# Kernel tuning notes

Measured on AMD Instinct MI355X. Metric: run time of the kernel, lower is better.

The kernel has to match this reference:

```python
import jax, jax.numpy as jnp
import numpy as np
import math

D_RES, N_HEADS, D_HEAD, D_MLP = 1024, 16, 64, 4096
EPS = 1e-5
IGNORE = -100000.0


def setup_inputs() -> dict:
    key = jax.random.key(0)
    ks = jax.random.split(key, 8)
    std = 0.02
    return {
        "resid_pre": jax.random.normal(ks[0], (2, 2048, D_RES), dtype=jnp.float32),
        "ln1_w": jnp.ones((D_RES,), jnp.float32),
        "ln1_b": jnp.zeros((D_RES,), jnp.float32),
        "W_Q": jax.random.normal(ks[1], (N_HEADS, D_RES, D_HEAD), jnp.float32) * std,
        "b_Q": jnp.zeros((N_HEADS, D_HEAD), jnp.float32),
        "W_K": jax.random.normal(ks[2], (N_HEADS, D_RES, D_HEAD), jnp.float32) * std,
        "b_K": jnp.zeros((N_HEADS, D_HEAD), jnp.float32),
        "W_V": jax.random.normal(ks[3], (N_HEADS, D_RES, D_HEAD), jnp.float32) * std,
        "b_V": jnp.zeros((N_HEADS, D_HEAD), jnp.float32),
        "W_O": jax.random.normal(ks[4], (N_HEADS, D_HEAD, D_RES), jnp.float32) * std,
        "b_O": jnp.zeros((D_RES,), jnp.float32),
        "ln2_w": jnp.ones((D_RES,), jnp.float32),
        "ln2_b": jnp.zeros((D_RES,), jnp.float32),
        "W_in": jax.random.normal(ks[5], (D_RES, D_MLP), jnp.float32) * std,
        "b_in": jnp.zeros((D_MLP,), jnp.float32),
        "W_out": jax.random.normal(ks[6], (D_MLP, D_RES), jnp.float32) * std,
        "b_out": jnp.zeros((D_RES,), jnp.float32),
    }


def _layernorm(x, w, b):
    x = x - jnp.mean(x, axis=-1, keepdims=True)
    scale = jnp.sqrt(jnp.mean(x * x, axis=-1, keepdims=True) + EPS)
    return (x / scale) * w + b


def reference(resid_pre, ln1_w, ln1_b, W_Q, b_Q, W_K, b_K, W_V, b_V, W_O, b_O,
              ln2_w, ln2_b, W_in, b_in, W_out, b_out):
    x = _layernorm(resid_pre, ln1_w, ln1_b)  # [b,s,d]
    q = jnp.einsum('bsd,hde->bshe', x, W_Q) + b_Q
    k = jnp.einsum('bsd,hde->bshe', x, W_K) + b_K
    v = jnp.einsum('bsd,hde->bshe', x, W_V) + b_V
    scores = jnp.einsum('bqhe,bkhe->bhqk', q, k) / math.sqrt(D_HEAD)
    S = scores.shape[-1]
    mask = jnp.triu(jnp.ones((S, S), dtype=bool), k=1)
    scores = jnp.where(mask, IGNORE, scores)
    pattern = jax.nn.softmax(scores, axis=-1)
    z = jnp.einsum('bhqk,bkhe->bqhe', pattern, v)
    attn_out = jnp.einsum('bqhe,hed->bqd', z, W_O) + b_O
    resid_mid = resid_pre + attn_out
    y = _layernorm(resid_mid, ln2_w, ln2_b)
    pre = jnp.einsum('bsd,dm->bsm', y, W_in) + b_in
    post = jax.nn.gelu(pre, approximate=False)
    mlp_out = jnp.einsum('bsm,md->bsd', post, W_out) + b_out
    return resid_mid + mlp_out
```

## Files before the change

kernel.cpp:

```cpp
#include <hip/hip_runtime.h>
#include <cstddef>

typedef unsigned short u16;
using short8 = __attribute__((ext_vector_type(8))) short;
using f32x4  = __attribute__((ext_vector_type(4))) float;

__device__ __forceinline__ float bf2f(u16 u) {
  union { unsigned int i; float f; } v; v.i = ((unsigned int)u) << 16; return v.f;
}
__device__ __forceinline__ u16 f2bf(float f) {
  __bf16 h = (__bf16)f;
  return __builtin_bit_cast(unsigned short, h);
}

__device__ __forceinline__ void load_lds16(const u16* g, u16* l) {
  __builtin_amdgcn_global_load_lds((const __attribute__((address_space(1))) void*)g,
                                   (__attribute__((address_space(3))) void*)l, 16, 0, 0);
}

__global__ __launch_bounds__(256) void transpose_k(const float* __restrict__ in,
                                                   u16* __restrict__ out,
                                                   int R, int C,
                                                   long inB, long outB) {
  __shared__ float tile[32][33];
  long zb = blockIdx.z;
  in  += zb * inB;
  out += zb * outB;
  int c0 = blockIdx.x * 32, r0 = blockIdx.y * 32;
  int tx = threadIdx.x, ty = threadIdx.y;
#pragma unroll
  for (int i = 0; i < 32; i += 8)
    tile[ty + i][tx] = in[(long)(r0 + ty + i) * C + c0 + tx];
  __syncthreads();
#pragma unroll
  for (int i = 0; i < 32; i += 8)
    out[(long)(c0 + ty + i) * R + r0 + tx] = f2bf(tile[tx][ty + i]);
}

__global__ __launch_bounds__(256) void transpose_v_k(const u16* __restrict__ qkv,
                                                     u16* __restrict__ vT) {
  __shared__ u16 tile[32][33];
  int bh = blockIdx.z;
  int b = bh >> 4, h = bh & 15;
  const u16* in = qkv + (size_t)b * 2048 * 3072 + 2048 + h * 64;
  u16* out = vT + (size_t)bh * 64 * 2048;
  int e0 = blockIdx.x * 32, s0 = blockIdx.y * 32;
  int tx = threadIdx.x, ty = threadIdx.y;
#pragma unroll
  for (int i = 0; i < 32; i += 8)
    tile[ty + i][tx] = in[(size_t)(s0 + ty + i) * 3072 + e0 + tx];
  __syncthreads();
#pragma unroll
  for (int i = 0; i < 32; i += 8)
    out[(size_t)(e0 + ty + i) * 2048 + s0 + tx] = tile[tx][ty + i];
}

__global__ void build_qkv_bias(const float* __restrict__ bQ, const float* __restrict__ bK,
                               const float* __restrict__ bV, float* __restrict__ out) {
  int i = blockIdx.x * 256 + threadIdx.x;
  float v;
  if (i < 1024) v = bQ[i];
  else if (i < 2048) v = bK[i - 1024];
  else v = bV[i - 2048];
  out[i] = v;
}

__global__ __launch_bounds__(256) void ln_k(const float* __restrict__ inp,
                                            const float* __restrict__ w,
                                            const float* __restrict__ bias,
                                            u16* __restrict__ out) {
  __shared__ float red[2][4];
  int row = blockIdx.x, t = threadIdx.x;
  int wave = t >> 6, lane = t & 63;
  size_t base = (size_t)row * 1024 + t * 4;
  float4 f = *(const float4*)(inp + base);
  float v[4] = {f.x, f.y, f.z, f.w};
  float s = v[0] + v[1] + v[2] + v[3];
#pragma unroll
  for (int off = 32; off; off >>= 1) s += __shfl_xor(s, off, 64);
  if (lane == 0) red[0][wave] = s;
  __syncthreads();
  float mean = (red[0][0] + red[0][1] + red[0][2] + red[0][3]) * (1.f / 1024.f);
  float c[4]; float sq = 0.f;
#pragma unroll
  for (int j = 0; j < 4; ++j) { c[j] = v[j] - mean; sq += c[j] * c[j]; }
#pragma unroll
  for (int off = 32; off; off >>= 1) sq += __shfl_xor(sq, off, 64);
  if (lane == 0) red[1][wave] = sq;
  __syncthreads();
  float var = (red[1][0] + red[1][1] + red[1][2] + red[1][3]) * (1.f / 1024.f);
  float inv = 1.f / sqrtf(var + 1e-5f);
  float4 wv = *(const float4*)(w + t * 4);
  float4 bv = *(const float4*)(bias + t * 4);
  out[base + 0] = f2bf(c[0] * inv * wv.x + bv.x);
  out[base + 1] = f2bf(c[1] * inv * wv.y + bv.y);
  out[base + 2] = f2bf(c[2] * inv * wv.z + bv.z);
  out[base + 3] = f2bf(c[3] * inv * wv.w + bv.w);
}

template<int TN, bool RESIDF, bool GELU, bool OUTF32>
__global__ __launch_bounds__(256, 2) void gemm_k(const u16* __restrict__ A,
                                                 const u16* __restrict__ BT,
                                                 const float* __restrict__ bias,
                                                 const float* __restrict__ resid,
                                                 void* __restrict__ Cout,
                                                 int M, int N, int K) {
  constexpr int NS = TN / 32;
  __shared__ u16 As[128 * 64];
  __shared__ u16 Bs[TN * 64];
  int n0 = blockIdx.x * TN, m0 = blockIdx.y * 128;
  int t = threadIdx.x;
  int wave = t >> 6, lane = t & 63;
  int wr = wave >> 1, wc = wave & 1;
  int ln16 = lane & 15, quad = lane >> 4;

  f32x4 acc[4][NS];
#pragma unroll
  for (int i = 0; i < 4; ++i)
#pragma unroll
    for (int j = 0; j < NS; ++j) acc[i][j] = (f32x4){0.f, 0.f, 0.f, 0.f};

  int lrow8 = lane >> 3;
  int gseg  = (lane & 7) ^ lrow8;
  const u16* aG = A  + (size_t)(m0 + wave * 8 + lrow8) * K + gseg * 8;
  const u16* bG = BT + (size_t)(n0 + wave * 8 + lrow8) * K + gseg * 8;
  u16* aL = As + wave * 8 * 64;
  u16* bL = Bs + wave * 8 * 64;

  int e = ln16 & 7;
  int arow = wr * 64 + ln16;
  int brow = wc * (TN / 2) + ln16;

  for (int k0 = 0; k0 < K; k0 += 64) {
    __syncthreads();
#pragma unroll
    for (int i = 0; i < 4; ++i)
      load_lds16(aG + (size_t)i * 32 * K + k0, aL + i * 32 * 64);
#pragma unroll
    for (int i = 0; i < TN / 32; ++i)
      load_lds16(bG + (size_t)i * 32 * K + k0, bL + i * 32 * 64);
    __syncthreads();
#pragma unroll
    for (int kk = 0; kk < 2; ++kk) {
      int slot = (kk * 4 + quad) ^ e;
      short8 af[4], bf[NS];
#pragma unroll
      for (int ms = 0; ms < 4; ++ms)
        af[ms] = *(const short8*)&As[(arow + ms * 16) * 64 + slot * 8];
#pragma unroll
      for (int ns = 0; ns < NS; ++ns)
        bf[ns] = *(const short8*)&Bs[(brow + ns * 16) * 64 + slot * 8];
#pragma unroll
      for (int ms = 0; ms < 4; ++ms)
#pragma unroll
        for (int ns = 0; ns < NS; ++ns)
          acc[ms][ns] = __builtin_amdgcn_mfma_f32_16x16x32_bf16(af[ms], bf[ns], acc[ms][ns], 0, 0, 0);
    }
  }

#pragma unroll
  for (int ms = 0; ms < 4; ++ms)
#pragma unroll
    for (int ns = 0; ns < NS; ++ns)
#pragma unroll
      for (int r = 0; r < 4; ++r) {
        int grow = m0 + wr * 64 + ms * 16 + quad * 4 + r;
        int gcol = n0 + wc * (TN / 2) + ns * 16 + ln16;
        size_t idx = (size_t)grow * N + gcol;
        float v = acc[ms][ns][r] + bias[gcol];
        if (GELU) v = 0.5f * v * (1.f + erff(v * 0.70710678118654752f));
        if (RESIDF) v += resid[idx];
        if (OUTF32) ((float*)Cout)[idx] = v;
        else        ((u16*)Cout)[idx] = f2bf(v);
      }
}

template<bool GELU>
__global__ __launch_bounds__(512, 2) void gemm256_k(const u16* __restrict__ A,
                                                    const u16* __restrict__ BT,
                                                    const float* __restrict__ bias,
                                                    u16* __restrict__ C,
                                                    int M, int N, int K) {
  constexpr int SLOT = 8192;
  __shared__ __align__(16) u16 As[4 * SLOT];
  __shared__ __align__(16) u16 Bs[4 * SLOT];
  int n0 = blockIdx.x * 256, m0 = blockIdx.y * 256;
  int t = threadIdx.x;
  int w = t >> 6, lane = t & 63;
  int wr = w >> 2, wc = w & 3;
  int ln16 = lane & 15, quad = lane >> 4;

  f32x4 acc[8][4];
#pragma unroll
  for (int i = 0; i < 8; ++i)
#pragma unroll
    for (int j = 0; j < 4; ++j) acc[i][j] = (f32x4){0.f, 0.f, 0.f, 0.f};

  const u16* aG0 = A  + (size_t)(m0 + w * 32 + (lane >> 2)) * K + (lane & 3) * 8;
  const u16* bG0 = BT + (size_t)(n0 + w * 32 + (lane >> 2)) * K + (lane & 3) * 8;
  u16* aL0 = As + w * 1024;
  u16* bL0 = Bs + w * 1024;

#define STAGE_A(j, tg) do {                                         \
    const u16* _g = aG0 + (size_t)(j) * 32;                         \
    u16* _l = aL0 + (tg) * SLOT;                                    \
    load_lds16(_g, _l);                                             \
    load_lds16(_g + (size_t)16 * K, _l + 512);                      \
  } while (0)
#define STAGE_B(j, tg) do {                                         \
    const u16* _g = bG0 + (size_t)(j) * 32;                         \
    u16* _l = bL0 + (tg) * SLOT;                                    \
    load_lds16(_g, _l);                                             \
    load_lds16(_g + (size_t)16 * K, _l + 512);                      \
  } while (0)

  STAGE_A(0, 0); STAGE_B(0, 0);
  STAGE_A(1, 1); STAGE_B(1, 1);
  STAGE_A(2, 2); STAGE_B(2, 2);
  asm volatile("s_waitcnt vmcnt(8)" ::: "memory");
  __builtin_amdgcn_s_barrier();

  int nslot = K >> 5;
  const u16* aRd = As + (wr * 128 + ln16) * 32 + quad * 8;
  const u16* bRd = Bs + (wc * 64  + ln16) * 32 + quad * 8;

  for (int s = 0; s < nslot; ++s) {
    int cur = s & 3, tgt = (s + 3) & 3;
    const u16* aB = aRd + cur * SLOT;
    const u16* bB = bRd + cur * SLOT;
    short8 a[4], b[4];

#pragma unroll
    for (int i = 0; i < 4; ++i) a[i] = *(const short8*)(aB + i * 512);
#pragma unroll
    for (int i = 0; i < 4; ++i) b[i] = *(const short8*)(bB + i * 512);
    if (s + 3 < nslot) STAGE_A(s + 3, tgt);
    __builtin_amdgcn_s_barrier();
    __builtin_amdgcn_s_setprio(1);
#pragma unroll
    for (int ms = 0; ms < 4; ++ms)
#pragma unroll
      for (int ns = 0; ns < 4; ++ns)
        acc[ms][ns] = __builtin_amdgcn_mfma_f32_16x16x32_bf16(a[ms], b[ns], acc[ms][ns], 0, 0, 0);
    __builtin_amdgcn_s_setprio(0);
    __builtin_amdgcn_s_barrier();

#pragma unroll
    for (int i = 0; i < 4; ++i) a[i] = *(const short8*)(aB + (4 + i) * 512);
    if (s + 3 < nslot) {
      STAGE_B(s + 3, tgt);
      asm volatile("s_waitcnt vmcnt(8)" ::: "memory");
    } else if (s + 2 < nslot) {
      asm volatile("s_waitcnt vmcnt(4)" ::: "memory");
    } else if (s + 1 < nslot) {
      asm volatile("s_waitcnt vmcnt(0)" ::: "memory");
    }
    __builtin_amdgcn_s_barrier();
    __builtin_amdgcn_s_setprio(1);
#pragma unroll
    for (int ms = 0; ms < 4; ++ms)
#pragma unroll
      for (int ns = 0; ns < 4; ++ns)
        acc[4 + ms][ns] = __builtin_amdgcn_mfma_f32_16x16x32_bf16(a[ms], b[ns], acc[4 + ms][ns], 0, 0, 0);
    __builtin_amdgcn_s_setprio(0);
    __builtin_amdgcn_s_barrier();
  }
#undef STAGE_A
#undef STAGE_B

#pragma unroll
  for (int ms = 0; ms < 8; ++ms)
#pragma unroll
    for (int ns = 0; ns < 4; ++ns) {
      int gcol = n0 + wc * 64 + ns * 16 + ln16;
      float bb = bias[gcol];
#pragma unroll
      for (int r = 0; r < 4; ++r) {
        int grow = m0 + wr * 128 + ms * 16 + quad * 4 + r;
        float v = acc[ms][ns][r] + bb;
        if (GELU) v = 0.5f * v * (1.f + erff(v * 0.70710678118654752f));
        C[(size_t)grow * N + gcol] = f2bf(v);
      }
    }
}

__global__ __launch_bounds__(512) void attn_k(const u16* __restrict__ qkv,
                                              const u16* __restrict__ vT,
                                              u16* __restrict__ z) {
  __shared__ __align__(16) u16 Ks[3 * 8192];
  __shared__ __align__(16) u16 Vs[3 * 8192];
  __shared__ __align__(16) u16 Ps[8 * 2048];
  int bh = blockIdx.x, p = blockIdx.y;
  int b = bh >> 4, h = bh & 15;
  int tA = p, tB = 15 - p;
  int t = threadIdx.x, w = t >> 6, lane = t & 63;
  int ln16 = lane & 15, quad = lane >> 4, e = ln16 & 7;

  short8 aq[2][2];
#pragma unroll
  for (int ti = 0; ti < 2; ++ti) {
    int tq = ti ? tB : tA;
    const u16* qrow = qkv + (size_t)(b * 2048 + tq * 128 + w * 16 + ln16) * 3072 + h * 64;
    aq[ti][0] = *(const short8*)(qrow + quad * 8);
    aq[ti][1] = *(const short8*)(qrow + 32 + quad * 8);
  }

  f32x4 zero4 = {0.f, 0.f, 0.f, 0.f};
  f32x4 o[2][4];
  float l_i[2][4];
#pragma unroll
  for (int ti = 0; ti < 2; ++ti)
#pragma unroll
    for (int n = 0; n < 4; ++n) { o[ti][n] = zero4; l_i[ti][n] = 0.f; }

  const u16* kB = qkv + (size_t)(b * 2048 + w * 16 + (lane >> 3)) * 3072
                + 1024 + h * 64 + (((lane & 7) ^ (lane >> 3))) * 8;
  const u16* vB0 = vT + ((size_t)(b * 16 + h) * 64 + w * 8 + (lane >> 4)) * 2048
                 + (((lane & 15) ^ (lane >> 4))) * 8;
  const u16* vB1 = vT + ((size_t)(b * 16 + h) * 64 + w * 8 + 4 + (lane >> 4)) * 2048
                 + (((lane & 15) ^ (4 + (lane >> 4)))) * 8;
  u16* kL = Ks + w * 16 * 64;
  u16* vL = Vs + w * 8 * 128;
  u16* psW = Ps + w * 2048;

#define STAGE(kt_, rg_) do {                                              \
    size_t kOff = (size_t)(kt_) * 128 * 3072;                             \
    u16* _kl = kL + (rg_) * 8192;                                         \
    load_lds16(kB + kOff, _kl);                                           \
    load_lds16(kB + kOff + (size_t)8 * 3072, _kl + 8 * 64);               \
    size_t vOff = (size_t)(kt_) * 128;                                    \
    u16* _vl = vL + (rg_) * 8192;                                         \
    load_lds16(vB0 + vOff, _vl);                                          \
    load_lds16(vB1 + vOff, _vl + 4 * 128);                                \
  } while (0)

  int nkt = tB + 1;
  STAGE(0, 0);

  for (int kt = 0; kt < nkt; ++kt) {
    int ring = kt % 3;
    if (kt + 1 < nkt) {
      STAGE(kt + 1, (kt + 1) % 3);
      asm volatile("s_waitcnt vmcnt(4)" ::: "memory");
    } else {
      asm volatile("s_waitcnt vmcnt(0)" ::: "memory");
    }
    __builtin_amdgcn_s_barrier();

    const u16* ks = Ks + ring * 8192;
    const u16* vs = Vs + ring * 8192;
    int kg = kt * 128;

#pragma unroll
    for (int ti = 0; ti < 2; ++ti) {
      int tq = ti ? tB : tA;
      if (kt > tq) continue;

      f32x4 s[8] = {zero4, zero4, zero4, zero4, zero4, zero4, zero4, zero4};
#pragma unroll
      for (int kk = 0; kk < 2; ++kk) {
        short8 a = aq[ti][kk];
        int slot = (kk * 4 + quad) ^ e;
#pragma unroll
        for (int n = 0; n < 8; ++n) {
          short8 kb = *(const short8*)&ks[(n * 16 + ln16) * 64 + slot * 8];
          s[n] = __builtin_amdgcn_mfma_f32_16x16x32_bf16(a, kb, s[n], 0, 0, 0);
        }
      }

      bool diag = (kt == tq);
      int qgb = tq * 128 + w * 16 + quad * 4;
#pragma unroll
      for (int r = 0; r < 4; ++r) {
        int q = quad * 4 + r, q7 = q & 7;
        int gq = qgb + r;
        float psum = 0.f;
#pragma unroll
        for (int n = 0; n < 8; ++n) {
          float pv = __expf(s[n][r] * 0.125f);
          if (diag && (kg + n * 16 + ln16 > gq)) pv = 0.f;
          psum += pv;
          psW[q * 128 + ((((n << 1) | (ln16 >> 3)) ^ q7) << 3) + e] = f2bf(pv);
        }
        l_i[ti][r] += psum;
      }

#pragma unroll
      for (int kk = 0; kk < 4; ++kk) {
        int slot = (kk * 4 + quad) ^ e;
        short8 ap = *(const short8*)&psW[ln16 * 128 + slot * 8];
#pragma unroll
        for (int n = 0; n < 4; ++n) {
          short8 bv = *(const short8*)&vs[(n * 16 + ln16) * 128 + slot * 8];
          o[ti][n] = __builtin_amdgcn_mfma_f32_16x16x32_bf16(ap, bv, o[ti][n], 0, 0, 0);
        }
      }
    }
  }
#undef STAGE

#pragma unroll
  for (int ti = 0; ti < 2; ++ti) {
    int tq = ti ? tB : tA;
    float inv[4];
#pragma unroll
    for (int r = 0; r < 4; ++r) {
      float sum = l_i[ti][r];
#pragma unroll
      for (int off = 8; off; off >>= 1) sum += __shfl_xor(sum, off, 16);
      inv[r] = 1.f / sum;
    }
#pragma unroll
    for (int n = 0; n < 4; ++n)
#pragma unroll
      for (int r = 0; r < 4; ++r)
        z[(size_t)(b * 2048 + tq * 128 + w * 16 + quad * 4 + r) * 1024
          + h * 64 + n * 16 + ln16] = f2bf(o[ti][n][r] * inv[r]);
  }
}

extern "C" void kernel_launch(void* const* d_in, const int* in_sizes, int n_in,
                              void* d_out, int out_size, void* d_ws, size_t ws_size,
                              hipStream_t stream) {
  const float* resid_pre = (const float*)d_in[0];
  const float* ln1_w = (const float*)d_in[1];
  const float* ln1_b = (const float*)d_in[2];
  const float* W_Q  = (const float*)d_in[3];
  const float* b_Q  = (const float*)d_in[4];
  const float* W_K  = (const float*)d_in[5];
  const float* b_K  = (const float*)d_in[6];
  const float* W_V  = (const float*)d_in[7];
  const float* b_V  = (const float*)d_in[8];
  const float* W_O  = (const float*)d_in[9];
  const float* b_O  = (const float*)d_in[10];
  const float* ln2_w = (const float*)d_in[11];
  const float* ln2_b = (const float*)d_in[12];
  const float* W_in  = (const float*)d_in[13];
  const float* b_in  = (const float*)d_in[14];
  const float* W_out = (const float*)d_in[15];
  const float* b_out = (const float*)d_in[16];
  float* out = (float*)d_out;

  char* w = (char*)d_ws;
  u16* WqkvT = (u16*)w;  w += (size_t)3072 * 1024 * 2;
  u16* WoT   = (u16*)w;  w += (size_t)1024 * 1024 * 2;
  u16* WinT  = (u16*)w;  w += (size_t)4096 * 1024 * 2;
  u16* WoutT = (u16*)w;  w += (size_t)1024 * 4096 * 2;
  float* qkvBias = (float*)w; w += 3072 * 4;
  u16* xln   = (u16*)w;  w += (size_t)4096 * 1024 * 2;
  float* resid_mid = (float*)w; w += (size_t)4096 * 1024 * 4;
  u16* qkvBuf = (u16*)w; w += (size_t)4096 * 3072 * 2;
  u16* zBuf  = (u16*)w;  w += (size_t)4096 * 1024 * 2;
  u16* vTBuf = (u16*)w;  w += (size_t)32 * 64 * 2048 * 2;
  u16* hBuf  = qkvBuf;

  dim3 tb(32, 8);
  transpose_k<<<dim3(2, 32, 16), tb, 0, stream>>>(W_Q, WqkvT,                1024, 64, 65536, 65536);
  transpose_k<<<dim3(2, 32, 16), tb, 0, stream>>>(W_K, WqkvT + 1024 * 1024,  1024, 64, 65536, 65536);
  transpose_k<<<dim3(2, 32, 16), tb, 0, stream>>>(W_V, WqkvT + 2048 * 1024,  1024, 64, 65536, 65536);
  transpose_k<<<dim3(32, 32, 1), tb, 0, stream>>>(W_O,  WoT,   1024, 1024, 0, 0);
  transpose_k<<<dim3(128, 32, 1), tb, 0, stream>>>(W_in, WinT,  1024, 4096, 0, 0);
  transpose_k<<<dim3(32, 128, 1), tb, 0, stream>>>(W_out, WoutT, 4096, 1024, 0, 0);
  build_qkv_bias<<<12, 256, 0, stream>>>(b_Q, b_K, b_V, qkvBias);

  ln_k<<<4096, 256, 0, stream>>>(resid_pre, ln1_w, ln1_b, xln);
  gemm256_k<false><<<dim3(12, 16), 512, 0, stream>>>(
      xln, WqkvT, qkvBias, qkvBuf, 4096, 3072, 1024);
  transpose_v_k<<<dim3(2, 64, 32), tb, 0, stream>>>(qkvBuf, vTBuf);
  attn_k<<<dim3(32, 8, 1), 512, 0, stream>>>(qkvBuf, vTBuf, zBuf);
  gemm_k<64, true, false, true><<<dim3(16, 32), 256, 0, stream>>>(
      zBuf, WoT, b_O, resid_pre, resid_mid, 4096, 1024, 1024);
  ln_k<<<4096, 256, 0, stream>>>(resid_mid, ln2_w, ln2_b, xln);
  gemm256_k<true><<<dim3(16, 16), 512, 0, stream>>>(
      xln, WinT, b_in, hBuf, 4096, 4096, 1024);
  gemm_k<64, true, false, true><<<dim3(16, 32), 256, 0, stream>>>(
      hBuf, WoutT, b_out, resid_mid, out, 4096, 1024, 4096);
}
```

Measured before the change: 365.1 us.

## Restructure 256x256 GEMM to double-buffered BK=64 tiles with XOR-swizzled LDS

Reworks the large GEMM's main loop. The old 4-slot ring with K-step 32 and split A/B staging becomes a 2-slot double buffer with K-step 64, one combined stage per iteration, and a single barrier pair per slot. The LDS row layout is XOR-swizzled to avoid bank conflicts when each lane reads 16-byte fragments. This halves the barrier count and the waitcnt bookkeeping per K element, but leaves only one tile of prefetch lookahead where there used to be three, which may expose global-load latency.

```diff
diff --git a/kernel.cpp b/kernel.cpp
--- a/kernel.cpp
+++ b/kernel.cpp
@@ -181,9 +181,9 @@
                                                     const float* __restrict__ bias,
                                                     u16* __restrict__ C,
                                                     int M, int N, int K) {
-  constexpr int SLOT = 8192;
-  __shared__ __align__(16) u16 As[4 * SLOT];
-  __shared__ __align__(16) u16 Bs[4 * SLOT];
+  constexpr int SLOT = 256 * 64;
+  __shared__ __align__(16) u16 As[2 * SLOT];
+  __shared__ __align__(16) u16 Bs[2 * SLOT];
   int n0 = blockIdx.x * 256, m0 = blockIdx.y * 256;
   int t = threadIdx.x;
   int w = t >> 6, lane = t & 63;
@@ -196,77 +196,67 @@
 #pragma unroll
     for (int j = 0; j < 4; ++j) acc[i][j] = (f32x4){0.f, 0.f, 0.f, 0.f};
 
-  const u16* aG0 = A  + (size_t)(m0 + w * 32 + (lane >> 2)) * K + (lane & 3) * 8;
-  const u16* bG0 = BT + (size_t)(n0 + w * 32 + (lane >> 2)) * K + (lane & 3) * 8;
-  u16* aL0 = As + w * 1024;
-  u16* bL0 = Bs + w * 1024;
-
-#define STAGE_A(j, tg) do {                                         \
-    const u16* _g = aG0 + (size_t)(j) * 32;                         \
-    u16* _l = aL0 + (tg) * SLOT;                                    \
-    load_lds16(_g, _l);                                             \
-    load_lds16(_g + (size_t)16 * K, _l + 512);                      \
+  int r8 = t >> 3;
+  int seg = (t & 7) ^ (r8 & 7);
+  const u16* aG0 = A  + (size_t)(m0 + r8) * K + seg * 8;
+  const u16* bG0 = BT + (size_t)(n0 + r8) * K + seg * 8;
+  u16* aLw = As + w * 512;
+  u16* bLw = Bs + w * 512;
+
+#define STAGE(s_, tg_) do {                                              \
+    const u16* _ga = aG0 + (size_t)(s_) * 64;                            \
+    const u16* _gb = bG0 + (size_t)(s_) * 64;                            \
+    u16* _la = aLw + (tg_) * SLOT;                                       \
+    u16* _lb = bLw + (tg_) * SLOT;                                       \
+    load_lds16(_ga,                       _la);                          \
+    load_lds16(_ga + (size_t)64 * K,      _la + 4096);                   \
+    load_lds16(_ga + (size_t)128 * K,     _la + 8192);                   \
+    load_lds16(_ga + (size_t)192 * K,     _la + 12288);                  \
+    load_lds16(_gb,                       _lb);                          \
+    load_lds16(_gb + (size_t)64 * K,      _lb + 4096);                   \
+    load_lds16(_gb + (size_t)128 * K,     _lb + 8192);                   \
+    load_lds16(_gb + (size_t)192 * K,     _lb + 12288);                  \
   } while (0)
-#define STAGE_B(j, tg) do {                                         \
-    const u16* _g = bG0 + (size_t)(j) * 32;                         \
-    u16* _l = bL0 + (tg) * SLOT;                                    \
-    load_lds16(_g, _l);                                             \
-    load_lds16(_g + (size_t)16 * K, _l + 512);                      \
-  } while (0)
-
-  STAGE_A(0, 0); STAGE_B(0, 0);
-  STAGE_A(1, 1); STAGE_B(1, 1);
-  STAGE_A(2, 2); STAGE_B(2, 2);
-  asm volatile("s_waitcnt vmcnt(8)" ::: "memory");
-  __builtin_amdgcn_s_barrier();
-
-  int nslot = K >> 5;
-  const u16* aRd = As + (wr * 128 + ln16) * 32 + quad * 8;
-  const u16* bRd = Bs + (wc * 64  + ln16) * 32 + quad * 8;
+
+  STAGE(0, 0);
+
+  int e = ln16 & 7;
+  int nslot = K >> 6;
+  const u16* aRd = As + (size_t)(wr * 128 + ln16) * 64;
+  const u16* bRd = Bs + (size_t)(wc * 64 + ln16) * 64;
 
   for (int s = 0; s < nslot; ++s) {
-    int cur = s & 3, tgt = (s + 3) & 3;
+    int cur = s & 1;
+    if (s + 1 < nslot) {
+      STAGE(s + 1, cur ^ 1);
+      asm volatile("s_waitcnt vmcnt(8)" ::: "memory");
+    } else {
+      asm volatile("s_waitcnt vmcnt(0)" ::: "memory");
+    }
+    __builtin_amdgcn_s_barrier();
+
     const u16* aB = aRd + cur * SLOT;
     const u16* bB = bRd + cur * SLOT;
-    short8 a[4], b[4];
-
-#pragma unroll
-    for (int i = 0; i < 4; ++i) a[i] = *(const short8*)(aB + i * 512);
-#pragma unroll
-    for (int i = 0; i < 4; ++i) b[i] = *(const short8*)(bB + i * 512);
-    if (s + 3 < nslot) STAGE_A(s + 3, tgt);
-    __builtin_amdgcn_s_barrier();
     __builtin_amdgcn_s_setprio(1);
 #pragma unroll
-    for (int ms = 0; ms < 4; ++ms)
+    for (int kk = 0; kk < 2; ++kk) {
+      int slot = (kk * 4 + quad) ^ e;
+      short8 bf[4];
 #pragma unroll
       for (int ns = 0; ns < 4; ++ns)
-        acc[ms][ns] = __builtin_amdgcn_mfma_f32_16x16x32_bf16(a[ms], b[ns], acc[ms][ns], 0, 0, 0);
-    __builtin_amdgcn_s_setprio(0);
-    __builtin_amdgcn_s_barrier();
-
-#pragma unroll
-    for (int i = 0; i < 4; ++i) a[i] = *(const short8*)(aB + (4 + i) * 512);
-    if (s + 3 < nslot) {
-      STAGE_B(s + 3, tgt);
-      asm volatile("s_waitcnt vmcnt(8)" ::: "memory");
-    } else if (s + 2 < nslot) {
-      asm volatile("s_waitcnt vmcnt(4)" ::: "memory");
-    } else if (s + 1 < nslot) {
-      asm volatile("s_waitcnt vmcnt(0)" ::: "memory");
-    }
-    __builtin_amdgcn_s_barrier();
-    __builtin_amdgcn_s_setprio(1);
-#pragma unroll
-    for (int ms = 0; ms < 4; ++ms)
-#pragma unroll
-      for (int ns = 0; ns < 4; ++ns)
-        acc[4 + ms][ns] = __builtin_amdgcn_mfma_f32_16x16x32_bf16(a[ms], b[ns], acc[4 + ms][ns], 0, 0, 0);
+        bf[ns] = *(const short8*)(bB + ns * 1024 + slot * 8);
+#pragma unroll
+      for (int ms = 0; ms < 8; ++ms) {
+        short8 af = *(const short8*)(aB + ms * 1024 + slot * 8);
+#pragma unroll
+        for (int ns = 0; ns < 4; ++ns)
+          acc[ms][ns] = __builtin_amdgcn_mfma_f32_16x16x32_bf16(af, bf[ns], acc[ms][ns], 0, 0, 0);
+      }
+    }
     __builtin_amdgcn_s_setprio(0);
     __builtin_amdgcn_s_barrier();
   }
-#undef STAGE_A
-#undef STAGE_B
+#undef STAGE
 
 #pragma unroll
   for (int ms = 0; ms < 8; ++ms)
```

After: 365.0 us. No clear change (-0.0%).
